# Optimization experiments

Measured on AMD Instinct MI355X. Metric: run time of the kernel, lower is better.

## Reference

```python
import jax, jax.numpy as jnp
import numpy as np

EPS = 1e-05
BITW = 8
BITA = 8


def _ste_round(v):
    # round with identity gradient (TF Round->Identity override)
    return v + jax.lax.stop_gradient(jnp.round(v) - v)


def _quantize_overflow(x, bits):
    # tensorlayer _quantize_overflow: linear quantization over [min, max]
    n = 2.0 ** bits - 1.0
    mx = jnp.max(x)
    mn = jnp.min(x)
    step = jax.lax.stop_gradient((mx - mn) / n)
    return _ste_round((x - mn) / step) * step + mn


def _conv2d_same(x, w):
    # x: [N,H,W,C], w: [KH,KW,C,F]
    return jax.lax.conv_general_dilated(
        x, w, window_strides=(1, 1), padding='SAME',
        dimension_numbers=('NHWC', 'HWIO', 'NHWC'))


def setup_inputs() -> dict:
    key = jax.random.key(0)
    k1, k2 = jax.random.split(key)
    x = jax.random.normal(k1, (32, 56, 56, 128), dtype=jnp.float32)
    W = jax.random.normal(k2, (3, 3, 128, 256), dtype=jnp.float32) * 0.02
    gamma = jnp.ones((256,), dtype=jnp.float32)
    beta = jnp.zeros((256,), dtype=jnp.float32)
    return {"x": x, "W": W, "gamma": gamma, "beta": beta}


def reference(x, W, gamma, beta):
    # 1) fake-quantize activations
    xq = _quantize_overflow(x, BITA)
    # 2) full-precision conv to get batch statistics (training path)
    conv_out = _conv2d_same(x, W)  # [N,H,W,F]
    mean = jnp.mean(conv_out, axis=(0, 1, 2))          # [F]
    var = jnp.var(conv_out, axis=(0, 1, 2))            # [F], biased (tf.nn.moments)
    inv_std = 1.0 / jnp.sqrt(var + EPS)                # [F]
    # 3) fold BN into weights/bias
    w_fold = W * (gamma * inv_std)                     # broadcast over [KH,KW,C,F]
    bias_fold = beta - gamma * mean * inv_std          # [F]
    # 4) quantize folded weights, conv with quantized activations
    wq = _quantize_overflow(w_fold, BITW)
    out = _conv2d_same(xq, wq) + bias_fold
    return jax.nn.relu(out)
```

## Files before the change

### kernel.cpp

```cpp
#include <hip/hip_runtime.h>

typedef float f32x4_t __attribute__((ext_vector_type(4)));
typedef __bf16 bf16x8_t __attribute__((ext_vector_type(8)));
typedef unsigned short u16x8_t __attribute__((ext_vector_type(8)));

#define NPIX        100352
#define PIX_PER_IMG 3136
#define PH          58
#define PPIX        3364
#define C_IN        128
#define C_OUT       256
#define NTAPS       9
#define NV4         3211264
#define NWELEM      294912
#define MBLK2       392
#define NPADPIX     107648

#define OFF_ENC     0
#define OFF_WQP     16
#define OFF_XQP     32
#define OFF_SCALE   64
#define OFF_BIAS    1152
#define OFF_WT      4096
#define OFF_WQT     593920
#define OFF_PSUM    1183744
#define OFF_PSQ     1986560
#define OFF_XPAD    2789376
#define OFF_XQPAD   30347264

__device__ __forceinline__ unsigned short f2bf(float x) {
  unsigned u = __float_as_uint(x);
  u += 0x7FFFu + ((u >> 16) & 1u);
  return (unsigned short)(u >> 16);
}
__device__ __forceinline__ unsigned encf(float v) {
  unsigned u = __float_as_uint(v);
  return (u & 0x80000000u) ? ~u : (u | 0x80000000u);
}
__device__ __forceinline__ float decf(unsigned e) {
  unsigned u = (e & 0x80000000u) ? (e ^ 0x80000000u) : ~e;
  return __uint_as_float(u);
}
__device__ __forceinline__ void gl_lds16(const void* g, void* l) {
  auto gp = (const __attribute__((address_space(1))) unsigned*)(const unsigned*)g;
  auto lp = (__attribute__((address_space(3))) unsigned*)(unsigned*)l;
  __builtin_amdgcn_global_load_lds(gp, lp, 16, 0, 0);
}

__global__ void kinit(unsigned* enc) {
  enc[0] = 0xFFFFFFFFu;
  enc[1] = 0u;
  enc[2] = 0xFFFFFFFFu;
  enc[3] = 0u;
}

__global__ void kminmax(const float4* __restrict__ x, unsigned* __restrict__ enc) {
  const int tid = blockIdx.x * blockDim.x + threadIdx.x;
  const int stride = gridDim.x * blockDim.x;
  float mn = 3.4e38f, mx = -3.4e38f;
  for (int i = tid; i < NV4; i += stride) {
    float4 v = x[i];
    mn = fminf(mn, fminf(fminf(v.x, v.y), fminf(v.z, v.w)));
    mx = fmaxf(mx, fmaxf(fmaxf(v.x, v.y), fmaxf(v.z, v.w)));
  }
  #pragma unroll
  for (int off = 32; off > 0; off >>= 1) {
    mn = fminf(mn, __shfl_xor(mn, off));
    mx = fmaxf(mx, __shfl_xor(mx, off));
  }
  __shared__ float smn[4], smx[4];
  const int lane = threadIdx.x & 63, w = threadIdx.x >> 6;
  if (lane == 0) { smn[w] = mn; smx[w] = mx; }
  __syncthreads();
  if (threadIdx.x == 0) {
    mn = fminf(fminf(smn[0], smn[1]), fminf(smn[2], smn[3]));
    mx = fmaxf(fmaxf(smx[0], smx[1]), fmaxf(smx[2], smx[3]));
    atomicMin(&enc[0], encf(mn));
    atomicMax(&enc[1], encf(mx));
  }
}

__global__ void kprep(const unsigned* __restrict__ enc, float* __restrict__ xqp) {
  const float mn = decf(enc[0]), mx = decf(enc[1]);
  xqp[0] = mn;
  xqp[1] = (mx - mn) / 255.0f;
  xqp[2] = 255.0f / (mx - mn);
}

__global__ void kwconv(const float* __restrict__ W, unsigned short* __restrict__ wt) {
  const int idx = blockIdx.x * 256 + threadIdx.x;
  if (idx >= NWELEM) return;
  const int c = idx & 127;
  const int f = (idx >> 7) & 255;
  const int tap = idx >> 15;
  wt[idx] = f2bf(W[(tap * 128 + c) * 256 + f]);
}

__global__ void kwq(const float* __restrict__ W, const float* __restrict__ scale,
                    const float* __restrict__ wqp, unsigned short* __restrict__ wqt) {
  const int idx = blockIdx.x * 256 + threadIdx.x;
  if (idx >= NWELEM) return;
  const int c = idx & 127;
  const int f = (idx >> 7) & 255;
  const int tap = idx >> 15;
  const float wmn = wqp[0], wstep = wqp[1], wrstep = wqp[2];
  const float v = W[(tap * 128 + c) * 256 + f] * scale[f];
  const float q = rintf((v - wmn) * wrstep) * wstep + wmn;
  wqt[idx] = f2bf(q);
}

__global__ void kpadfill(const float* __restrict__ x, const float* __restrict__ xqp,
                         unsigned short* __restrict__ xpad, unsigned short* __restrict__ xqpad)
{
  const int tid = blockIdx.x * 256 + threadIdx.x;
  if (tid >= NPADPIX * 16) return;
  const int pp = tid >> 4;
  const int c8 = (tid & 15) << 3;
  const int n = pp / PPIX;
  const int rem = pp - n * PPIX;
  const int hp = rem / PH;
  const int wp = rem - hp * PH;
  u16x8_t vb, vq;
  #pragma unroll
  for (int j = 0; j < 8; ++j) { vb[j] = 0; vq[j] = 0; }
  if (hp >= 1 && hp <= 56 && wp >= 1 && wp <= 56) {
    const float mn = xqp[0], step = xqp[1], rstep = xqp[2];
    const float* src = x + ((n * PIX_PER_IMG) + (hp - 1) * 56 + (wp - 1)) * C_IN + c8;
    const float4 a = *(const float4*)src;
    const float4 b = *(const float4*)(src + 4);
    const float v[8] = {a.x, a.y, a.z, a.w, b.x, b.y, b.z, b.w};
    #pragma unroll
    for (int j = 0; j < 8; ++j) {
      vb[j] = f2bf(v[j]);
      const float qv = rintf((v[j] - mn) * rstep) * step + mn;
      vq[j] = f2bf(qv);
    }
  }
  *(u16x8_t*)(xpad + pp * C_IN + c8) = vb;
  *(u16x8_t*)(xqpad + pp * C_IN + c8) = vq;
}

template<int STATS>
__global__ __launch_bounds__(512, 2)
void kconv(const unsigned short* __restrict__ xin,
           const unsigned short* __restrict__ wt,
           float* __restrict__ out,
           const float* __restrict__ bias,
           float* __restrict__ psum,
           float* __restrict__ psq)
{
  const int l = blockIdx.x;
  const int xcd = l & 7, k = l >> 3;
  const int bn = k & 1;
  const int bm = xcd * 49 + (k >> 1);

  const int tid = threadIdx.x;
  const int lane = tid & 63;
  const int wid = tid >> 6;
  const int wm = wid >> 1;
  const int wn = wid & 1;
  const int l16 = lane & 15;
  const int rsub = lane >> 4;

  __shared__ __align__(16) unsigned char smem[98304];

  const int lrow = lane >> 3;
  const int lchunk = (lane & 7) ^ lrow;
  unsigned aoff[4];
  #pragma unroll
  for (int r = 0; r < 4; ++r) {
    const int pix = bm * 256 + r * 64 + wid * 8 + lrow;
    const int n = pix / PIX_PER_IMG;
    const int rem = pix - n * PIX_PER_IMG;
    const int hh = rem / 56;
    const int ww = rem - hh * 56;
    aoff[r] = (unsigned)((n * PPIX + hh * PH + ww) * C_IN + lchunk * 8);
  }
  unsigned boff[2];
  #pragma unroll
  for (int r = 0; r < 2; ++r) {
    const int f = bn * 128 + r * 64 + wid * 8 + lrow;
    boff[r] = (unsigned)(f * C_IN + lchunk * 8);
  }

  f32x4_t acc[4][4];
  #pragma unroll
  for (int im = 0; im < 4; ++im)
    #pragma unroll
    for (int in = 0; in < 4; ++in)
      #pragma unroll
      for (int j = 0; j < 4; ++j) acc[im][in][j] = 0.f;

  auto stage = [&](int bsel, int s) {
    const int tap = s >> 1, h = (s & 1) << 6;
    const int kh = tap / 3, kw = tap - kh * 3;
    const unsigned atap = (unsigned)((kh * PH + kw) * C_IN + h);
    const unsigned btap = (unsigned)(tap * C_OUT * C_IN + h);
    unsigned char* sA = smem + bsel * 49152;
    unsigned char* sB = sA + 32768;
    #pragma unroll
    for (int r = 0; r < 4; ++r)
      gl_lds16(xin + atap + aoff[r], sA + r * 8192 + wid * 1024);
    #pragma unroll
    for (int r = 0; r < 2; ++r)
      gl_lds16(wt + btap + boff[r], sB + r * 8192 + wid * 1024);
  };

  stage(0, 0);
  __syncthreads();
  int cur = 0;

  #pragma unroll 1
  for (int s = 0; s < 18; ++s) {
    if (s < 17) stage(cur ^ 1, s + 1);
    const unsigned char* sA = smem + cur * 49152;
    const unsigned char* sB = sA + 32768;
    #pragma unroll
    for (int kb = 0; kb < 2; ++kb) {
      const int c = kb * 4 + rsub;
      const int p = c ^ (l16 & 7);
      bf16x8_t av[4], bv[4];
      #pragma unroll
      for (int im = 0; im < 4; ++im)
        av[im] = *(const bf16x8_t*)(sA + (wm * 64 + im * 16 + l16) * 128 + p * 16);
      #pragma unroll
      for (int in = 0; in < 4; ++in)
        bv[in] = *(const bf16x8_t*)(sB + (wn * 64 + in * 16 + l16) * 128 + p * 16);
      #pragma unroll
      for (int im = 0; im < 4; ++im)
        #pragma unroll
        for (int in = 0; in < 4; ++in)
          acc[im][in] = __builtin_amdgcn_mfma_f32_16x16x32_bf16(av[im], bv[in], acc[im][in], 0, 0, 0);
    }
    __syncthreads();
    cur ^= 1;
  }

  if (STATS) {
    float* sb = (float*)smem;
    #pragma unroll
    for (int in = 0; in < 4; ++in) {
      float s = 0.f, q = 0.f;
      #pragma unroll
      for (int im = 0; im < 4; ++im)
        #pragma unroll
        for (int j = 0; j < 4; ++j) {
          const float v = acc[im][in][j];
          s += v; q += v * v;
        }
      s += __shfl_xor(s, 16); q += __shfl_xor(q, 16);
      s += __shfl_xor(s, 32); q += __shfl_xor(q, 32);
      if (lane < 16) {
        sb[wid * 64 + in * 16 + lane] = s;
        sb[512 + wid * 64 + in * 16 + lane] = q;
      }
    }
    __syncthreads();
    if (tid < 128) {
      const int wn2 = tid >> 6, cl = tid & 63;
      float s = 0.f, q = 0.f;
      #pragma unroll
      for (int wm2 = 0; wm2 < 4; ++wm2) {
        s += sb[(wm2 * 2 + wn2) * 64 + cl];
        q += sb[512 + (wm2 * 2 + wn2) * 64 + cl];
      }
      const int b = bm * 2 + bn;
      psum[b * 128 + tid] = s;
      psq[b * 128 + tid] = q;
    }
  } else {
    float bval[4];
    #pragma unroll
    for (int in = 0; in < 4; ++in)
      bval[in] = bias[bn * 128 + wn * 64 + in * 16 + l16];
    #pragma unroll
    for (int im = 0; im < 4; ++im) {
      #pragma unroll
      for (int j = 0; j < 4; ++j) {
        const int pix = bm * 256 + wm * 64 + im * 16 + rsub * 4 + j;
        #pragma unroll
        for (int in = 0; in < 4; ++in) {
          const int f = bn * 128 + wn * 64 + in * 16 + l16;
          out[pix * 256 + f] = fmaxf(acc[im][in][j] + bval[in], 0.f);
        }
      }
    }
  }
}

__global__ __launch_bounds__(256)
void kstats(const float* __restrict__ psum, const float* __restrict__ psq,
            const float* __restrict__ gamma, const float* __restrict__ beta,
            float* __restrict__ scale, float* __restrict__ bias)
{
  const int ch = blockIdx.x;
  const int bn = ch >> 7, col = ch & 127;
  float s = 0.f, q = 0.f;
  for (int bm = threadIdx.x; bm < MBLK2; bm += 256) {
    const int b = bm * 2 + bn;
    s += psum[b * 128 + col];
    q += psq[b * 128 + col];
  }
  #pragma unroll
  for (int off = 32; off > 0; off >>= 1) {
    s += __shfl_xor(s, off);
    q += __shfl_xor(q, off);
  }
  __shared__ float ss[4], sq2[4];
  const int lane = threadIdx.x & 63, w = threadIdx.x >> 6;
  if (lane == 0) { ss[w] = s; sq2[w] = q; }
  __syncthreads();
  if (threadIdx.x == 0) {
    s = ss[0] + ss[1] + ss[2] + ss[3];
    q = sq2[0] + sq2[1] + sq2[2] + sq2[3];
    const float inv = 1.0f / (float)NPIX;
    const float mean = s * inv;
    const float var = q * inv - mean * mean;
    const float istd = 1.0f / sqrtf(var + 1e-5f);
    const float g = gamma[ch];
    scale[ch] = g * istd;
    bias[ch] = beta[ch] - g * mean * istd;
  }
}

__global__ __launch_bounds__(256)
void kwmm(const float* __restrict__ W, const float* __restrict__ scale,
          unsigned* __restrict__ enc)
{
  const int idx = blockIdx.x * 256 + threadIdx.x;
  float v = 0.f;
  if (idx < NWELEM) v = W[idx] * scale[idx & 255];
  float mn = v, mx = v;
  #pragma unroll
  for (int off = 32; off > 0; off >>= 1) {
    mn = fminf(mn, __shfl_xor(mn, off));
    mx = fmaxf(mx, __shfl_xor(mx, off));
  }
  __shared__ float rmn[4], rmx[4];
  const int lane = threadIdx.x & 63, w = threadIdx.x >> 6;
  if (lane == 0) { rmn[w] = mn; rmx[w] = mx; }
  __syncthreads();
  if (threadIdx.x == 0) {
    mn = fminf(fminf(rmn[0], rmn[1]), fminf(rmn[2], rmn[3]));
    mx = fmaxf(fmaxf(rmx[0], rmx[1]), fmaxf(rmx[2], rmx[3]));
    atomicMin(&enc[2], encf(mn));
    atomicMax(&enc[3], encf(mx));
  }
}

__global__ void kwprep(const unsigned* __restrict__ enc, float* __restrict__ wqp) {
  const float mn = decf(enc[2]), mx = decf(enc[3]);
  wqp[0] = mn;
  wqp[1] = (mx - mn) / 255.0f;
  wqp[2] = 255.0f / (mx - mn);
}

extern "C" void kernel_launch(void* const* d_in, const int* in_sizes, int n_in,
                              void* d_out, int out_size, void* d_ws, size_t ws_size,
                              hipStream_t stream)
{
  const float* x     = (const float*)d_in[0];
  const float* W     = (const float*)d_in[1];
  const float* gamma = (const float*)d_in[2];
  const float* beta  = (const float*)d_in[3];
  float* out = (float*)d_out;
  char* ws = (char*)d_ws;

  unsigned* enc        = (unsigned*)(ws + OFF_ENC);
  float* wqp           = (float*)(ws + OFF_WQP);
  float* xqp           = (float*)(ws + OFF_XQP);
  float* scale         = (float*)(ws + OFF_SCALE);
  float* bias          = (float*)(ws + OFF_BIAS);
  unsigned short* Wt   = (unsigned short*)(ws + OFF_WT);
  unsigned short* Wqt  = (unsigned short*)(ws + OFF_WQT);
  float* psum          = (float*)(ws + OFF_PSUM);
  float* psq           = (float*)(ws + OFF_PSQ);
  unsigned short* xpad  = (unsigned short*)(ws + OFF_XPAD);
  unsigned short* xqpad = (unsigned short*)(ws + OFF_XQPAD);

  kinit<<<1, 64, 0, stream>>>(enc);
  kminmax<<<1024, 256, 0, stream>>>((const float4*)x, enc);
  kprep<<<1, 64, 0, stream>>>(enc, xqp);
  kwconv<<<1152, 256, 0, stream>>>(W, Wt);
  kpadfill<<<6728, 256, 0, stream>>>(x, xqp, xpad, xqpad);
  kconv<1><<<784, 512, 0, stream>>>(xpad, Wt, nullptr, nullptr, psum, psq);
  kstats<<<256, 256, 0, stream>>>(psum, psq, gamma, beta, scale, bias);
  kwmm<<<1152, 256, 0, stream>>>(W, scale, enc);
  kwprep<<<1, 64, 0, stream>>>(enc, wqp);
  kwq<<<1152, 256, 0, stream>>>(W, scale, wqp, Wqt);
  kconv<0><<<784, 512, 0, stream>>>(xqpad, Wqt, out, bias, nullptr, nullptr);
}
```

Baseline: 243.5 us.

## Widen conv tile to full 256 output channels with deeper async pipeline

The implicit-GEMM conv kernel now computes a 256x256 tile (all output channels) per block instead of 256x128, so each activation tile is loaded once rather than twice and the grid halves to 392 blocks. The K loop is restructured with two stages in flight, explicit vmcnt waits and raw barriers fenced by sched_barrier, to overlap global-to-LDS loads with MFMA work. The tiny kprep/kwprep kernels are removed and their scalar math is folded into the consuming kernels, saving launches. In exchange, LDS use grows to 128KB and accumulator registers double, which limits occupancy to one block per CU, and 392 blocks may leave CUs unevenly loaded.

```diff
diff --git a/kernel.cpp b/kernel.cpp
--- a/kernel.cpp
+++ b/kernel.cpp
@@ -13,12 +13,10 @@
 #define NTAPS       9
 #define NV4         3211264
 #define NWELEM      294912
-#define MBLK2       392
+#define MTILES      392
 #define NPADPIX     107648
 
 #define OFF_ENC     0
-#define OFF_WQP     16
-#define OFF_XQP     32
 #define OFF_SCALE   64
 #define OFF_BIAS    1152
 #define OFF_WT      4096
@@ -46,6 +44,7 @@
   auto lp = (__attribute__((address_space(3))) unsigned*)(unsigned*)l;
   __builtin_amdgcn_global_load_lds(gp, lp, 16, 0, 0);
 }
+#define SCHED_FENCE() __builtin_amdgcn_sched_barrier(0)
 
 __global__ void kinit(unsigned* enc) {
   enc[0] = 0xFFFFFFFFu;
@@ -80,13 +79,6 @@
   }
 }
 
-__global__ void kprep(const unsigned* __restrict__ enc, float* __restrict__ xqp) {
-  const float mn = decf(enc[0]), mx = decf(enc[1]);
-  xqp[0] = mn;
-  xqp[1] = (mx - mn) / 255.0f;
-  xqp[2] = 255.0f / (mx - mn);
-}
-
 __global__ void kwconv(const float* __restrict__ W, unsigned short* __restrict__ wt) {
   const int idx = blockIdx.x * 256 + threadIdx.x;
   if (idx >= NWELEM) return;
@@ -97,19 +89,21 @@
 }
 
 __global__ void kwq(const float* __restrict__ W, const float* __restrict__ scale,
-                    const float* __restrict__ wqp, unsigned short* __restrict__ wqt) {
+                    const unsigned* __restrict__ enc, unsigned short* __restrict__ wqt) {
   const int idx = blockIdx.x * 256 + threadIdx.x;
   if (idx >= NWELEM) return;
   const int c = idx & 127;
   const int f = (idx >> 7) & 255;
   const int tap = idx >> 15;
-  const float wmn = wqp[0], wstep = wqp[1], wrstep = wqp[2];
+  const float wmn = decf(enc[2]), wmx = decf(enc[3]);
+  const float wstep = (wmx - wmn) / 255.0f;
+  const float wrstep = 255.0f / (wmx - wmn);
   const float v = W[(tap * 128 + c) * 256 + f] * scale[f];
   const float q = rintf((v - wmn) * wrstep) * wstep + wmn;
   wqt[idx] = f2bf(q);
 }
 
-__global__ void kpadfill(const float* __restrict__ x, const float* __restrict__ xqp,
+__global__ void kpadfill(const float* __restrict__ x, const unsigned* __restrict__ enc,
                          unsigned short* __restrict__ xpad, unsigned short* __restrict__ xqpad)
 {
   const int tid = blockIdx.x * 256 + threadIdx.x;
@@ -124,7 +118,8 @@
   #pragma unroll
   for (int j = 0; j < 8; ++j) { vb[j] = 0; vq[j] = 0; }
   if (hp >= 1 && hp <= 56 && wp >= 1 && wp <= 56) {
-    const float mn = xqp[0], step = xqp[1], rstep = xqp[2];
+    const float mn = decf(enc[0]), mx = decf(enc[1]);
+    const float step = (mx - mn) / 255.0f, rstep = 255.0f / (mx - mn);
     const float* src = x + ((n * PIX_PER_IMG) + (hp - 1) * 56 + (wp - 1)) * C_IN + c8;
     const float4 a = *(const float4*)src;
     const float4 b = *(const float4*)(src + 4);
@@ -149,92 +144,104 @@
            float* __restrict__ psum,
            float* __restrict__ psq)
 {
-  const int l = blockIdx.x;
-  const int xcd = l & 7, k = l >> 3;
-  const int bn = k & 1;
-  const int bm = xcd * 49 + (k >> 1);
+  const int bid = blockIdx.x;
+  const int bm = (bid & 7) * 49 + (bid >> 3);
 
   const int tid = threadIdx.x;
   const int lane = tid & 63;
   const int wid = tid >> 6;
-  const int wm = wid >> 1;
-  const int wn = wid & 1;
+  const int wm = wid >> 2;
+  const int wn = wid & 3;
   const int l16 = lane & 15;
   const int rsub = lane >> 4;
 
-  __shared__ __align__(16) unsigned char smem[98304];
-
-  const int lrow = lane >> 3;
-  const int lchunk = (lane & 7) ^ lrow;
+  __shared__ __align__(16) unsigned char smem[131072];
+
+  const int lchunk = (tid & 7) ^ ((tid >> 3) & 7);
+
   unsigned aoff[4];
   #pragma unroll
-  for (int r = 0; r < 4; ++r) {
-    const int pix = bm * 256 + r * 64 + wid * 8 + lrow;
+  for (int j = 0; j < 4; ++j) {
+    const int pix = bm * 256 + j * 64 + (tid >> 3);
     const int n = pix / PIX_PER_IMG;
     const int rem = pix - n * PIX_PER_IMG;
     const int hh = rem / 56;
     const int ww = rem - hh * 56;
-    aoff[r] = (unsigned)((n * PPIX + hh * PH + ww) * C_IN + lchunk * 8);
-  }
-  unsigned boff[2];
-  #pragma unroll
-  for (int r = 0; r < 2; ++r) {
-    const int f = bn * 128 + r * 64 + wid * 8 + lrow;
-    boff[r] = (unsigned)(f * C_IN + lchunk * 8);
-  }
-
-  f32x4_t acc[4][4];
-  #pragma unroll
-  for (int im = 0; im < 4; ++im)
+    aoff[j] = (unsigned)((n * PPIX + hh * PH + ww) * C_IN + lchunk * 8);
+  }
+  unsigned boff[4];
+  #pragma unroll
+  for (int j = 0; j < 4; ++j) {
+    const int f = j * 64 + (tid >> 3);
+    boff[j] = (unsigned)(f * C_IN + lchunk * 8);
+  }
+
+  f32x4_t acc[8][4];
+  #pragma unroll
+  for (int im = 0; im < 8; ++im)
     #pragma unroll
     for (int in = 0; in < 4; ++in)
       #pragma unroll
       for (int j = 0; j < 4; ++j) acc[im][in][j] = 0.f;
 
   auto stage = [&](int bsel, int s) {
-    const int tap = s >> 1, h = (s & 1) << 6;
+    const int tap = s >> 1;
+    const int chalf = (s & 1) << 6;
     const int kh = tap / 3, kw = tap - kh * 3;
-    const unsigned atap = (unsigned)((kh * PH + kw) * C_IN + h);
-    const unsigned btap = (unsigned)(tap * C_OUT * C_IN + h);
-    unsigned char* sA = smem + bsel * 49152;
+    const unsigned atap = (unsigned)((kh * PH + kw) * C_IN + chalf);
+    const unsigned btap = (unsigned)(tap * C_OUT * C_IN + chalf);
+    unsigned char* sA = smem + bsel * 65536;
     unsigned char* sB = sA + 32768;
     #pragma unroll
-    for (int r = 0; r < 4; ++r)
-      gl_lds16(xin + atap + aoff[r], sA + r * 8192 + wid * 1024);
-    #pragma unroll
-    for (int r = 0; r < 2; ++r)
-      gl_lds16(wt + btap + boff[r], sB + r * 8192 + wid * 1024);
+    for (int j = 0; j < 4; ++j)
+      gl_lds16(xin + atap + aoff[j], sA + j * 8192 + wid * 1024);
+    #pragma unroll
+    for (int j = 0; j < 4; ++j)
+      gl_lds16(wt + btap + boff[j], sB + j * 8192 + wid * 1024);
   };
 
-  stage(0, 0);
-  __syncthreads();
-  int cur = 0;
-
-  #pragma unroll 1
-  for (int s = 0; s < 18; ++s) {
-    if (s < 17) stage(cur ^ 1, s + 1);
-    const unsigned char* sA = smem + cur * 49152;
+  auto compute = [&](int bsel) {
+    const unsigned char* sA = smem + bsel * 65536;
     const unsigned char* sB = sA + 32768;
     #pragma unroll
-    for (int kb = 0; kb < 2; ++kb) {
-      const int c = kb * 4 + rsub;
+    for (int ks = 0; ks < 2; ++ks) {
+      const int c = ks * 4 + rsub;
       const int p = c ^ (l16 & 7);
-      bf16x8_t av[4], bv[4];
-      #pragma unroll
-      for (int im = 0; im < 4; ++im)
-        av[im] = *(const bf16x8_t*)(sA + (wm * 64 + im * 16 + l16) * 128 + p * 16);
+      bf16x8_t av[8], bv[4];
+      #pragma unroll
+      for (int im = 0; im < 8; ++im)
+        av[im] = *(const bf16x8_t*)(sA + (wm * 128 + im * 16 + l16) * 128 + p * 16);
       #pragma unroll
       for (int in = 0; in < 4; ++in)
         bv[in] = *(const bf16x8_t*)(sB + (wn * 64 + in * 16 + l16) * 128 + p * 16);
       #pragma unroll
-      for (int im = 0; im < 4; ++im)
+      for (int im = 0; im < 8; ++im)
         #pragma unroll
         for (int in = 0; in < 4; ++in)
           acc[im][in] = __builtin_amdgcn_mfma_f32_16x16x32_bf16(av[im], bv[in], acc[im][in], 0, 0, 0);
     }
-    __syncthreads();
-    cur ^= 1;
-  }
+  };
+
+  stage(0, 0);
+  stage(1, 1);
+
+  #pragma unroll 1
+  for (int t = 0; t < 17; ++t) {
+    asm volatile("s_waitcnt vmcnt(8)" ::: "memory");
+    SCHED_FENCE();
+    __builtin_amdgcn_s_barrier();
+    SCHED_FENCE();
+    compute(t & 1);
+    SCHED_FENCE();
+    __builtin_amdgcn_s_barrier();
+    SCHED_FENCE();
+    if (t < 16) stage(t & 1, t + 2);
+  }
+  asm volatile("s_waitcnt vmcnt(0)" ::: "memory");
+  SCHED_FENCE();
+  __builtin_amdgcn_s_barrier();
+  SCHED_FENCE();
+  compute(1);
 
   if (STATS) {
     float* sb = (float*)smem;
@@ -242,7 +249,7 @@
     for (int in = 0; in < 4; ++in) {
       float s = 0.f, q = 0.f;
       #pragma unroll
-      for (int im = 0; im < 4; ++im)
+      for (int im = 0; im < 8; ++im)
         #pragma unroll
         for (int j = 0; j < 4; ++j) {
           const float v = acc[im][in][j];
@@ -256,31 +263,26 @@
       }
     }
     __syncthreads();
-    if (tid < 128) {
+    if (tid < 256) {
       const int wn2 = tid >> 6, cl = tid & 63;
-      float s = 0.f, q = 0.f;
-      #pragma unroll
-      for (int wm2 = 0; wm2 < 4; ++wm2) {
-        s += sb[(wm2 * 2 + wn2) * 64 + cl];
-        q += sb[512 + (wm2 * 2 + wn2) * 64 + cl];
-      }
-      const int b = bm * 2 + bn;
-      psum[b * 128 + tid] = s;
-      psq[b * 128 + tid] = q;
+      const float s = sb[wn2 * 64 + cl] + sb[(4 + wn2) * 64 + cl];
+      const float q = sb[512 + wn2 * 64 + cl] + sb[512 + (4 + wn2) * 64 + cl];
+      psum[bm * 256 + tid] = s;
+      psq[bm * 256 + tid] = q;
     }
   } else {
     float bval[4];
     #pragma unroll
     for (int in = 0; in < 4; ++in)
-      bval[in] = bias[bn * 128 + wn * 64 + in * 16 + l16];
-    #pragma unroll
-    for (int im = 0; im < 4; ++im) {
+      bval[in] = bias[wn * 64 + in * 16 + l16];
+    #pragma unroll
+    for (int im = 0; im < 8; ++im) {
       #pragma unroll
       for (int j = 0; j < 4; ++j) {
-        const int pix = bm * 256 + wm * 64 + im * 16 + rsub * 4 + j;
+        const int pix = bm * 256 + wm * 128 + im * 16 + rsub * 4 + j;
         #pragma unroll
         for (int in = 0; in < 4; ++in) {
-          const int f = bn * 128 + wn * 64 + in * 16 + l16;
+          const int f = wn * 64 + in * 16 + l16;
           out[pix * 256 + f] = fmaxf(acc[im][in][j] + bval[in], 0.f);
         }
       }
@@ -294,12 +296,10 @@
             float* __restrict__ scale, float* __restrict__ bias)
 {
   const int ch = blockIdx.x;
-  const int bn = ch >> 7, col = ch & 127;
   float s = 0.f, q = 0.f;
-  for (int bm = threadIdx.x; bm < MBLK2; bm += 256) {
-    const int b = bm * 2 + bn;
-    s += psum[b * 128 + col];
-    q += psq[b * 128 + col];
+  for (int bm = threadIdx.x; bm < MTILES; bm += 256) {
+    s += psum[bm * 256 + ch];
+    q += psq[bm * 256 + ch];
   }
   #pragma unroll
   for (int off = 32; off > 0; off >>= 1) {
@@ -348,13 +348,6 @@
   }
 }
 
-__global__ void kwprep(const unsigned* __restrict__ enc, float* __restrict__ wqp) {
-  const float mn = decf(enc[2]), mx = decf(enc[3]);
-  wqp[0] = mn;
-  wqp[1] = (mx - mn) / 255.0f;
-  wqp[2] = 255.0f / (mx - mn);
-}
-
 extern "C" void kernel_launch(void* const* d_in, const int* in_sizes, int n_in,
                               void* d_out, int out_size, void* d_ws, size_t ws_size,
                               hipStream_t stream)
@@ -367,8 +360,6 @@
   char* ws = (char*)d_ws;
 
   unsigned* enc        = (unsigned*)(ws + OFF_ENC);
-  float* wqp           = (float*)(ws + OFF_WQP);
-  float* xqp           = (float*)(ws + OFF_XQP);
   float* scale         = (float*)(ws + OFF_SCALE);
   float* bias          = (float*)(ws + OFF_BIAS);
   unsigned short* Wt   = (unsigned short*)(ws + OFF_WT);
@@ -380,13 +371,11 @@
 
   kinit<<<1, 64, 0, stream>>>(enc);
   kminmax<<<1024, 256, 0, stream>>>((const float4*)x, enc);
-  kprep<<<1, 64, 0, stream>>>(enc, xqp);
   kwconv<<<1152, 256, 0, stream>>>(W, Wt);
-  kpadfill<<<6728, 256, 0, stream>>>(x, xqp, xpad, xqpad);
-  kconv<1><<<784, 512, 0, stream>>>(xpad, Wt, nullptr, nullptr, psum, psq);
+  kpadfill<<<6728, 256, 0, stream>>>(x, enc, xpad, xqpad);
+  kconv<1><<<MTILES, 512, 0, stream>>>(xpad, Wt, nullptr, nullptr, psum, psq);
   kstats<<<256, 256, 0, stream>>>(psum, psq, gamma, beta, scale, bias);
   kwmm<<<1152, 256, 0, stream>>>(W, scale, enc);
-  kwprep<<<1, 64, 0, stream>>>(enc, wqp);
-  kwq<<<1152, 256, 0, stream>>>(W, scale, wqp, Wqt);
-  kconv<0><<<784, 512, 0, stream>>>(xqpad, Wqt, out, bias, nullptr, nullptr);
-}
+  kwq<<<1152, 256, 0, stream>>>(W, scale, enc, Wqt);
+  kconv<0><<<MTILES, 512, 0, stream>>>(xqpad, Wqt, out, bias, nullptr, nullptr);
+}
```

After: 230.4 us. 1.06x faster.
